# Performance work log

Measured on AMD Instinct MI355X. Metric: run time of the kernel, lower is better.

The kernel has to match this reference:

```python
import jax, jax.numpy as jnp
import numpy as np

K = 8          # opt.pk, explicit precision cutoff
MARGIN = 0.2   # opt.margin
NEG = -1e30    # sentinel for masked sort keys


def setup_inputs() -> dict:
    key = jax.random.key(0)
    k1, k2 = jax.random.split(key)
    batch_reprs = jax.random.normal(k1, (4096, 512), dtype=jnp.float32)
    batch_labels = jax.random.randint(k2, (4096,), 0, 64)
    return {"batch_reprs": batch_reprs, "batch_labels": batch_labels}


def _forward(batch_reprs, batch_labels):
    B = batch_reprs.shape[0]
    dt = batch_reprs.dtype
    # cls_match_mat: 1 if same class
    match = (batch_labels[:, None] == batch_labels[None, :]).astype(dt)
    # pairwise euclidean distance (squared=False), safe sqrt at zero diagonal
    sq = jnp.sum(batch_reprs * batch_reprs, axis=1)
    res = jnp.maximum(sq[:, None] - 2.0 * (batch_reprs @ batch_reprs.T) + sq[None, :], 0.0)
    zero = res <= 0.0
    d = jnp.where(zero, 0.0, jnp.sqrt(jnp.where(zero, 1.0, res)))
    sim_hat = -d + (1.0 - match) * MARGIN  # use_margin=True path
    # rank via double argsort (descending similarity -> rank 1 = best)
    order = jnp.argsort(-sim_hat, axis=1)
    rank = jnp.argsort(order, axis=1).astype(dt) + 1.0
    pos_nums = jnp.sum(match, axis=1)
    ks = jnp.minimum(pos_nums, jnp.asarray(K + 1, dt))[:, None]  # k_mat per row
    w = 1.0 / jnp.log2(rank + 1.0) + 1.0  # DCG-style rank weight
    # false positives: not same class, within top-k_i
    fp_mask = (match < 1.0) & (rank <= ks)
    fp_nums = jnp.sum(fp_mask, axis=1)  # |N| per row
    # false negatives: same class, beyond top-k_i
    fn_mask = (match > 0.0) & (rank > ks)
    fp_term = jnp.sum(jnp.where(fp_mask, sim_hat * w, 0.0))
    # per-row variable-size topk over false negatives, vectorized:
    # mask non-FN entries to -inf, sort desc, keep first fp_nums[i] entries
    fn_key = jnp.where(fn_mask, sim_hat, NEG)
    fn_order = jnp.argsort(-fn_key, axis=1)
    sorted_sim = jnp.take_along_axis(sim_hat, fn_order, axis=1)
    sorted_w = jnp.take_along_axis(w, fn_order, axis=1)
    sorted_valid = jnp.take_along_axis(fn_mask, fn_order, axis=1)
    take = (jnp.arange(B)[None, :].astype(dt) < fp_nums[:, None]) & sorted_valid
    fn_term = jnp.sum(jnp.where(take, sorted_sim * sorted_w, 0.0))
    # rows with fp_num==0 contribute 0 to both terms, matching the host loop
    return fp_term - fn_term


def reference(batch_reprs, batch_labels):
    return _forward(batch_reprs, batch_labels)
```

## Files before the change

### kernel.cpp

```cpp
#include <hip/hip_runtime.h>
#include <math.h>

#define BB 4096
#define DD 512
#define KTOP 9
#define MARGIN_F 0.2f
#define NT 32
#define NTRI (NT * (NT + 1) / 2)

typedef __attribute__((ext_vector_type(8))) short short8;
typedef __attribute__((ext_vector_type(4))) float f32x4;
typedef unsigned long long u64;

__device__ unsigned short g_Rhi[(size_t)BB * DD];
__device__ u64 g_cmask[64 * 64];

__device__ __forceinline__ unsigned short f2bf(float x) {
  unsigned u = __float_as_uint(x);
  u += 0x7fffu + ((u >> 16) & 1u);
  return (unsigned short)(u >> 16);
}

__device__ __forceinline__ float ord16val(unsigned o16) {
  unsigned e = (o16 << 16) | 0x8000u;
  unsigned s = (e & 0x80000000u) ? (e ^ 0x80000000u) : ~e;
  return __uint_as_float(s);
}

__device__ __forceinline__ unsigned wavemax32_dpp(unsigned c) {
#define MSTEP(CTRL, RM)                                                        \
  {                                                                            \
    unsigned o = (unsigned)__builtin_amdgcn_update_dpp(0, (int)c, CTRL, RM, 0xf, false); \
    if (o > c) c = o;                                                          \
  }
  MSTEP(0xB1, 0xf) MSTEP(0x4E, 0xf) MSTEP(0x141, 0xf) MSTEP(0x140, 0xf)
  MSTEP(0x142, 0xa) MSTEP(0x143, 0xc)
#undef MSTEP
  return (unsigned)__builtin_amdgcn_readlane((int)c, 63);
}

__device__ __forceinline__ int wavesum_dpp(int c) {
#define SSTEP(CTRL, RM)                                                        \
  c += __builtin_amdgcn_update_dpp(0, c, CTRL, RM, 0xf, false);
  SSTEP(0xB1, 0xf) SSTEP(0x4E, 0xf) SSTEP(0x141, 0xf) SSTEP(0x140, 0xf)
  SSTEP(0x142, 0xa) SSTEP(0x143, 0xc)
#undef SSTEP
  return __builtin_amdgcn_readlane(c, 63);
}

__device__ __forceinline__ unsigned u4c(const uint4& f, int q) {
  return q == 0 ? f.x : q == 1 ? f.y : q == 2 ? f.z : f.w;
}

__global__ __launch_bounds__(64) void splitsq(const float* __restrict__ R,
                                              float* __restrict__ sq) {
  const int row = blockIdx.x, lane = threadIdx.x;
  const float4* r4 = (const float4*)(R + (size_t)row * DD);
  float4 a = r4[lane], b = r4[lane + 64];
  float xs[8] = {a.x, a.y, a.z, a.w, b.x, b.y, b.z, b.w};
  unsigned short hs[8];
  float s = 0.f;
  #pragma unroll
  for (int q = 0; q < 8; ++q) {
    float x = xs[q];
    s += x * x;
    hs[q] = f2bf(x);
  }
  const size_t base = (size_t)row * DD;
  *(ushort4*)&g_Rhi[base + lane * 4]       = *(ushort4*)&hs[0];
  *(ushort4*)&g_Rhi[base + 256 + lane * 4] = *(ushort4*)&hs[4];
  #pragma unroll
  for (int off = 32; off; off >>= 1) s += __shfl_down(s, off);
  if (lane == 0) sq[row] = s;
}

__global__ __launch_bounds__(64) void buildmask(const int* __restrict__ labels) {
  __shared__ int slab[BB];
  const int c = blockIdx.x, lane = threadIdx.x;
  for (int i = lane; i < BB / 4; i += 64) ((int4*)slab)[i] = ((const int4*)labels)[i];
  __syncthreads();
  u64 m = 0;
  #pragma unroll
  for (int e = 0; e < 64; ++e) {
    int j = 512 * (e >> 3) + 8 * lane + (e & 7);
    m |= (u64)(slab[j] == c) << e;
  }
  g_cmask[c * 64 + lane] = m;
}

__global__ __launch_bounds__(256, 2) void simgemm_rs2(const int* __restrict__ labels,
                                                      const float* __restrict__ sq,
                                                      unsigned short* __restrict__ simq) {
  const int x = blockIdx.x & 7;
  int c = blockIdx.x >> 3;
  int bi = 0, bj = 0;
  #pragma unroll
  for (int q = 0; q < 4; ++q) {
    const int bjq = (q < 2) ? (2 * x + q) : (28 - 2 * x + q);
    const int n = bjq + 1;
    if (c >= 0 && c < n) { bj = bjq; bi = c; }
    c -= n;
  }
  const int i0 = bi * 128, j0 = bj * 128;

  __shared__ __align__(16) unsigned char smembytes[65536];
  unsigned short (*kbuf)[2][8192] = (unsigned short (*)[2][8192])smembytes;

  const int tid = threadIdx.x;
  const int wid = tid >> 6, lane = tid & 63;
  const int wr = wid >> 1, wc = wid & 1;
  const int lrow = lane & 15, kblk = lane >> 4;

  const int sr = lane & 15;
  const int sc = (lane >> 4) * 8;
  const int r0 = (2 * wid + 0) * 16 + sr;
  const int r1 = (2 * wid + 1) * 16 + sr;
  const unsigned short* gA0 = &g_Rhi[(size_t)(i0 + r0) * DD + sc];
  const unsigned short* gA1 = &g_Rhi[(size_t)(i0 + r1) * DD + sc];
  const unsigned short* gB0 = &g_Rhi[(size_t)(j0 + r0) * DD + sc];
  const unsigned short* gB1 = &g_Rhi[(size_t)(j0 + r1) * DD + sc];

  f32x4 acc[4][4] = {};
  uint4 vA00, vA01, vA10, vA11, vB00, vB01, vB10, vB11;

#define STAGE_LOAD(K0)                                                         \
  vA00 = *(const uint4*)(gA0 + (K0));      vB00 = *(const uint4*)(gB0 + (K0)); \
  vA01 = *(const uint4*)(gA0 + (K0) + 32); vB01 = *(const uint4*)(gB0 + (K0) + 32); \
  vA10 = *(const uint4*)(gA1 + (K0));      vB10 = *(const uint4*)(gB1 + (K0)); \
  vA11 = *(const uint4*)(gA1 + (K0) + 32); vB11 = *(const uint4*)(gB1 + (K0) + 32);

#define STAGE_WRITE(BUF)                                                       \
  {                                                                            \
    const int c0 = (2 * wid + 0) * 1024 + lane * 8;                            \
    const int c1 = (2 * wid + 1) * 1024 + lane * 8;                            \
    *(uint4*)&kbuf[BUF][0][c0]       = vA00; *(uint4*)&kbuf[BUF][1][c0]       = vB00; \
    *(uint4*)&kbuf[BUF][0][c0 + 512] = vA01; *(uint4*)&kbuf[BUF][1][c0 + 512] = vB01; \
    *(uint4*)&kbuf[BUF][0][c1]       = vA10; *(uint4*)&kbuf[BUF][1][c1]       = vB10; \
    *(uint4*)&kbuf[BUF][0][c1 + 512] = vA11; *(uint4*)&kbuf[BUF][1][c1 + 512] = vB11; \
  }

  STAGE_LOAD(0);
  STAGE_WRITE(0);
  STAGE_LOAD(64);
  __syncthreads();

  for (int step = 0; step < 8; ++step) {
    const int cur = step & 1;

    #pragma unroll
    for (int kk = 0; kk < 2; ++kk) {
      short8 a[4], b[4];
      #pragma unroll
      for (int m = 0; m < 4; ++m)
        a[m] = *(const short8*)&kbuf[cur][0][(wr * 4 + m) * 1024 + kk * 512 + lane * 8];
      #pragma unroll
      for (int n = 0; n < 4; ++n)
        b[n] = *(const short8*)&kbuf[cur][1][(wc * 4 + n) * 1024 + kk * 512 + lane * 8];
      #pragma unroll
      for (int m = 0; m < 4; ++m) {
        #pragma unroll
        for (int n = 0; n < 4; ++n) {
          acc[m][n] = __builtin_amdgcn_mfma_f32_16x16x32_bf16(a[m], b[n], acc[m][n], 0, 0, 0);
        }
      }
    }

    if (step < 7) {
      STAGE_WRITE(cur ^ 1);
      if (step < 6) { STAGE_LOAD((step + 2) * 64); }
      __syncthreads();
    }
  }
#undef STAGE_LOAD
#undef STAGE_WRITE

  __syncthreads();
  unsigned short (*T)[132] = (unsigned short (*)[132])smembytes;
  float* sqi = (float*)(smembytes + 33792);
  float* sqj = (float*)(smembytes + 34304);
  int* labi  = (int*)(smembytes + 34816);
  int* labj  = (int*)(smembytes + 35328);
  if (tid < 128) { sqi[tid] = sq[i0 + tid]; labi[tid] = labels[i0 + tid]; }
  else { int t2 = tid - 128; sqj[t2] = sq[j0 + t2]; labj[t2] = labels[j0 + t2]; }
  __syncthreads();

  #pragma unroll
  for (int m = 0; m < 4; ++m) {
    const int rbase = wr * 64 + m * 16 + kblk * 4;
    #pragma unroll
    for (int n = 0; n < 4; ++n) {
      const int ccol = wc * 64 + n * 16 + lrow;
      const float sqc = sqj[ccol];
      const int lc_ = labj[ccol];
      #pragma unroll
      for (int reg = 0; reg < 4; ++reg) {
        const int r = rbase + reg;
        float res = sqi[r] - 2.0f * acc[m][n][reg] + sqc;
        float dd = (res <= 0.f) ? 0.f : sqrtf(res);
        float sv = -dd + ((labi[r] != lc_) ? MARGIN_F : 0.f);
        unsigned su = __float_as_uint(sv);
        unsigned ord = su ^ ((unsigned)((int)su >> 31) | 0x80000000u);
        T[r][ccol] = (unsigned short)(ord >> 16);
      }
    }
  }
  __syncthreads();

  const int srow0 = tid >> 4, scol0 = (tid & 15) * 8;
  #pragma unroll
  for (int p = 0; p < 8; ++p) {
    const int r = p * 16 + srow0;
    short8 w = *(const short8*)&T[r][scol0];
    *(short8*)&simq[(size_t)(i0 + r) * BB + j0 + scol0] = w;
  }
  if (bi != bj) {
    #pragma unroll
    for (int p = 0; p < 8; ++p) {
      const int col = p * 16 + srow0;
      unsigned short tmp[8];
      #pragma unroll
      for (int t = 0; t < 8; ++t) tmp[t] = T[scol0 + t][col];
      *(short8*)&simq[(size_t)(j0 + col) * BB + i0 + scol0] = *(short8*)tmp;
    }
  }
}

#define TOP2UPD(k, a, b) {                                                     \
  unsigned _mx = ((k) > (a)) ? (k) : (a);                                      \
  unsigned _mn = ((k) > (a)) ? (a) : (k);                                      \
  (a) = _mx;                                                                   \
  (b) = (_mn > (b)) ? _mn : (b); }

__global__ __launch_bounds__(128) void rowproc9(const unsigned short* __restrict__ simq,
                                                const int* __restrict__ labels,
                                                float* __restrict__ partials) {
  __shared__ unsigned sred[2 * KTOP + 2][2];
  __shared__ int sint[2 + 2 * KTOP];

  const int tid = threadIdx.x;
  const int lane = tid & 63;
  const int h = tid >> 6;
  const int row = blockIdx.x;

  const uint4* rp = (const uint4*)(simq + (size_t)row * BB);
  uint4 w0 = rp[lane + (4 * h + 0) * 64];
  uint4 w1 = rp[lane + (4 * h + 1) * 64];
  uint4 w2 = rp[lane + (4 * h + 2) * 64];
  uint4 w3 = rp[lane + (4 * h + 3) * 64];

  const int myl = labels[row];
  const unsigned mh = (unsigned)(g_cmask[myl * 64 + lane] >> (32 * h));
  const unsigned lbase2 = (unsigned)((4095 - 8 * lane) << 1);

  unsigned k[32];
  #pragma unroll
  for (int s = 0; s < 4; ++s) {
    const uint4 w = s == 0 ? w0 : s == 1 ? w1 : s == 2 ? w2 : w3;
    const unsigned base_s = lbase2 - (unsigned)(1024 * (4 * h + s));
    #pragma unroll
    for (int q = 0; q < 4; ++q) {
      const unsigned wv = u4c(w, q);
      const int e0 = s * 8 + q * 2;
      k[e0]     = ((wv & 0xffffu) << 13)
                | (base_s - (unsigned)((q * 2) << 1)     + ((mh >> e0) & 1u));
      k[e0 + 1] = ((wv >> 16) << 13)
                | (base_s - (unsigned)((q * 2 + 1) << 1) + ((mh >> (e0 + 1)) & 1u));
    }
  }

  {
    int p = wavesum_dpp(__popc(mh));
    sint[h] = p;
  }
  __syncthreads();
  const int pos = sint[0] + sint[1];
  const int ks = min(pos, KTOP);

  unsigned h1 = 0, h2 = 0;
  #pragma unroll
  for (int e = 0; e < 32; ++e) TOP2UPD(k[e], h1, h2);

  unsigned kth = 0;
  float fp = 0.f; int fpn = 0;
  #pragma unroll
  for (int t = 0; t < KTOP; ++t) {
    if (t < ks) {
      sred[t][h] = wavemax32_dpp(h1);
    }
    __syncthreads();
    if (t < ks) {
      const unsigned g = max(sred[t][0], sred[t][1]);
      if (!(g & 1u)) { fp += ord16val(g >> 13) * (1.f / log2f((float)(t + 2)) + 1.f); fpn++; }
      if (t == ks - 1) kth = g;
      if (h1 == g) {
        h1 = h2; h2 = ~0u;
        if (h1 == ~0u) {
          h1 = 0; h2 = 0;
          #pragma unroll
          for (int e = 0; e < 32; ++e) {
            if (k[e] < g) TOP2UPD(k[e], h1, h2);
          }
        }
      }
    }
  }

  float fn = 0.f;
  if (fpn > 0) {
    unsigned f1 = 0, f2 = 0;
    #pragma unroll
    for (int e = 0; e < 32; ++e) {
      if ((k[e] & 1u) && k[e] < kth) TOP2UPD(k[e], f1, f2);
    }
    unsigned ck[KTOP];
    int nc = 0;
    #pragma unroll
    for (int u = 0; u < KTOP; ++u) {
      ck[u] = ~0u;
      if (u < fpn) {
        sred[KTOP + 1 + u][h] = wavemax32_dpp(f1);
      }
      __syncthreads();
      if (u < fpn) {
        const unsigned g = max(sred[KTOP + 1 + u][0], sred[KTOP + 1 + u][1]);
        if (g != 0u) {
          ck[u] = g; nc = u + 1;
          if (f1 == g) {
            f1 = f2; f2 = ~0u;
            if (f1 == ~0u) {
              f1 = 0; f2 = 0;
              #pragma unroll
              for (int e = 0; e < 32; ++e) {
                if ((k[e] & 1u) && k[e] < g) TOP2UPD(k[e], f1, f2);
              }
            }
          }
        }
      }
    }
    if (nc > 0) {
      int cnt[KTOP];
      #pragma unroll
      for (int u = 0; u < KTOP; ++u) cnt[u] = 0;
      #pragma unroll
      for (int e = 0; e < 32; ++e) {
        #pragma unroll
        for (int u = 0; u < KTOP; ++u) cnt[u] += (k[e] > ck[u]) ? 1 : 0;
      }
      #pragma unroll
      for (int u = 0; u < KTOP; ++u) {
        sint[2 + h * KTOP + u] = wavesum_dpp(cnt[u]);
      }
    }
    __syncthreads();
    if (nc > 0) {
      #pragma unroll
      for (int u = 0; u < KTOP; ++u) {
        if (u < nc) {
          const int rank = 1 + sint[2 + u] + sint[2 + KTOP + u];
          fn += ord16val(ck[u] >> 13) * (1.f / log2f((float)(rank + 1)) + 1.f);
        }
      }
    }
  }

  if (tid == 0) partials[row] = fp - fn;
}

__global__ __launch_bounds__(256) void finalreduce(const float* __restrict__ partials,
                                                   float* __restrict__ out) {
  __shared__ float s[256];
  const int tid = threadIdx.x;
  float acc = 0.f;
  for (int j = tid; j < BB; j += 256) acc += partials[j];
  s[tid] = acc; __syncthreads();
  #pragma unroll
  for (int st = 128; st; st >>= 1) { if (tid < st) s[tid] += s[tid + st]; __syncthreads(); }
  if (tid == 0) out[0] = s[0];
}

extern "C" void kernel_launch(void* const* d_in, const int* in_sizes, int n_in,
                              void* d_out, int out_size, void* d_ws, size_t ws_size,
                              hipStream_t stream) {
  const float* R      = (const float*)d_in[0];
  const int*   labels = (const int*)d_in[1];
  float* out = (float*)d_out;

  unsigned short* simq = (unsigned short*)d_ws;
  float* sq            = (float*)((char*)d_ws + (size_t)BB * BB * 2);
  float* partials      = sq + BB;

  splitsq<<<BB, 64, 0, stream>>>(R, sq);
  buildmask<<<64, 64, 0, stream>>>(labels);
  simgemm_rs2<<<NTRI, 256, 0, stream>>>(labels, sq, simq);
  rowproc9<<<BB, 128, 0, stream>>>(simq, labels, partials);
  finalreduce<<<1, 256, 0, stream>>>(partials, out);
}
```

Before: 93.06 us.

## Repack bf16 operands into MFMA fragment layout and load GEMM operands directly from global

Adds a repack kernel that rewrites the bf16 matrix into per-16-row blocks already laid out as MFMA fragments. The similarity GEMM then reads its fragments straight from global memory (cached in L2) with register double-buffering, dropping the LDS staging, the double-buffered shared tiles and the per-step barriers. Shared memory per block shrinks to the size the epilogue needs. The cost is an extra kernel launch and a full extra pass over the bf16 copy, plus reliance on cache hits for operands that are reused across tiles.

```diff
diff --git a/kernel.cpp b/kernel.cpp
--- a/kernel.cpp
+++ b/kernel.cpp
@@ -13,6 +13,7 @@
 typedef unsigned long long u64;
 
 __device__ unsigned short g_Rhi[(size_t)BB * DD];
+__device__ unsigned short g_Rpk[(size_t)BB * DD];
 __device__ u64 g_cmask[64 * 64];
 
 __device__ __forceinline__ unsigned short f2bf(float x) {
@@ -74,6 +75,19 @@
   if (lane == 0) sq[row] = s;
 }
 
+__global__ __launch_bounds__(256) void repack(void) {
+  const int p = blockIdx.x;
+  #pragma unroll
+  for (int i = 0; i < 4; ++i) {
+    const int idx = i * 256 + threadIdx.x;
+    const int ks = idx >> 6, l = idx & 63;
+    const int row = p * 16 + (l & 15);
+    const int k0 = ks * 32 + (l >> 4) * 8;
+    *(uint4*)&g_Rpk[(size_t)p * 8192 + (size_t)idx * 8] =
+        *(const uint4*)&g_Rhi[(size_t)row * DD + k0];
+  }
+}
+
 __global__ __launch_bounds__(64) void buildmask(const int* __restrict__ labels) {
   __shared__ int slab[BB];
   const int c = blockIdx.x, lane = threadIdx.x;
@@ -88,9 +102,9 @@
   g_cmask[c * 64 + lane] = m;
 }
 
-__global__ __launch_bounds__(256, 2) void simgemm_rs2(const int* __restrict__ labels,
-                                                      const float* __restrict__ sq,
-                                                      unsigned short* __restrict__ simq) {
+__global__ __launch_bounds__(256, 2) void simgemm_pk(const int* __restrict__ labels,
+                                                     const float* __restrict__ sq,
+                                                     unsigned short* __restrict__ simq) {
   const int x = blockIdx.x & 7;
   int c = blockIdx.x >> 3;
   int bi = 0, bj = 0;
@@ -103,78 +117,50 @@
   }
   const int i0 = bi * 128, j0 = bj * 128;
 
-  __shared__ __align__(16) unsigned char smembytes[65536];
-  unsigned short (*kbuf)[2][8192] = (unsigned short (*)[2][8192])smembytes;
+  __shared__ __align__(16) unsigned char smembytes[35840];
 
   const int tid = threadIdx.x;
   const int wid = tid >> 6, lane = tid & 63;
   const int wr = wid >> 1, wc = wid & 1;
   const int lrow = lane & 15, kblk = lane >> 4;
 
-  const int sr = lane & 15;
-  const int sc = (lane >> 4) * 8;
-  const int r0 = (2 * wid + 0) * 16 + sr;
-  const int r1 = (2 * wid + 1) * 16 + sr;
-  const unsigned short* gA0 = &g_Rhi[(size_t)(i0 + r0) * DD + sc];
-  const unsigned short* gA1 = &g_Rhi[(size_t)(i0 + r1) * DD + sc];
-  const unsigned short* gB0 = &g_Rhi[(size_t)(j0 + r0) * DD + sc];
-  const unsigned short* gB1 = &g_Rhi[(size_t)(j0 + r1) * DD + sc];
+  const unsigned short* pA[4];
+  const unsigned short* pB[4];
+  #pragma unroll
+  for (int m = 0; m < 4; ++m) {
+    pA[m] = g_Rpk + (size_t)(bi * 8 + wr * 4 + m) * 8192 + lane * 8;
+    pB[m] = g_Rpk + (size_t)(bj * 8 + wc * 4 + m) * 8192 + lane * 8;
+  }
 
   f32x4 acc[4][4] = {};
-  uint4 vA00, vA01, vA10, vA11, vB00, vB01, vB10, vB11;
-
-#define STAGE_LOAD(K0)                                                         \
-  vA00 = *(const uint4*)(gA0 + (K0));      vB00 = *(const uint4*)(gB0 + (K0)); \
-  vA01 = *(const uint4*)(gA0 + (K0) + 32); vB01 = *(const uint4*)(gB0 + (K0) + 32); \
-  vA10 = *(const uint4*)(gA1 + (K0));      vB10 = *(const uint4*)(gB1 + (K0)); \
-  vA11 = *(const uint4*)(gA1 + (K0) + 32); vB11 = *(const uint4*)(gB1 + (K0) + 32);
-
-#define STAGE_WRITE(BUF)                                                       \
-  {                                                                            \
-    const int c0 = (2 * wid + 0) * 1024 + lane * 8;                            \
-    const int c1 = (2 * wid + 1) * 1024 + lane * 8;                            \
-    *(uint4*)&kbuf[BUF][0][c0]       = vA00; *(uint4*)&kbuf[BUF][1][c0]       = vB00; \
-    *(uint4*)&kbuf[BUF][0][c0 + 512] = vA01; *(uint4*)&kbuf[BUF][1][c0 + 512] = vB01; \
-    *(uint4*)&kbuf[BUF][0][c1]       = vA10; *(uint4*)&kbuf[BUF][1][c1]       = vB10; \
-    *(uint4*)&kbuf[BUF][0][c1 + 512] = vA11; *(uint4*)&kbuf[BUF][1][c1 + 512] = vB11; \
-  }
-
-  STAGE_LOAD(0);
-  STAGE_WRITE(0);
-  STAGE_LOAD(64);
-  __syncthreads();
-
-  for (int step = 0; step < 8; ++step) {
+  short8 fa[2][4], fb[2][4];
+
+  #pragma unroll
+  for (int m = 0; m < 4; ++m) {
+    fa[0][m] = *(const short8*)(pA[m]);
+    fb[0][m] = *(const short8*)(pB[m]);
+  }
+
+  #pragma unroll
+  for (int step = 0; step < 16; ++step) {
     const int cur = step & 1;
-
-    #pragma unroll
-    for (int kk = 0; kk < 2; ++kk) {
-      short8 a[4], b[4];
-      #pragma unroll
-      for (int m = 0; m < 4; ++m)
-        a[m] = *(const short8*)&kbuf[cur][0][(wr * 4 + m) * 1024 + kk * 512 + lane * 8];
-      #pragma unroll
-      for (int n = 0; n < 4; ++n)
-        b[n] = *(const short8*)&kbuf[cur][1][(wc * 4 + n) * 1024 + kk * 512 + lane * 8];
+    if (step < 15) {
+      const int koff = (step + 1) * 512;
       #pragma unroll
       for (int m = 0; m < 4; ++m) {
-        #pragma unroll
-        for (int n = 0; n < 4; ++n) {
-          acc[m][n] = __builtin_amdgcn_mfma_f32_16x16x32_bf16(a[m], b[n], acc[m][n], 0, 0, 0);
-        }
-      }
-    }
-
-    if (step < 7) {
-      STAGE_WRITE(cur ^ 1);
-      if (step < 6) { STAGE_LOAD((step + 2) * 64); }
-      __syncthreads();
-    }
-  }
-#undef STAGE_LOAD
-#undef STAGE_WRITE
-
-  __syncthreads();
+        fa[cur ^ 1][m] = *(const short8*)(pA[m] + koff);
+        fb[cur ^ 1][m] = *(const short8*)(pB[m] + koff);
+      }
+    }
+    #pragma unroll
+    for (int m = 0; m < 4; ++m) {
+      #pragma unroll
+      for (int n = 0; n < 4; ++n) {
+        acc[m][n] = __builtin_amdgcn_mfma_f32_16x16x32_bf16(fa[cur][m], fb[cur][n], acc[m][n], 0, 0, 0);
+      }
+    }
+  }
+
   unsigned short (*T)[132] = (unsigned short (*)[132])smembytes;
   float* sqi = (float*)(smembytes + 33792);
   float* sqj = (float*)(smembytes + 34304);
@@ -391,8 +377,9 @@
   float* partials      = sq + BB;
 
   splitsq<<<BB, 64, 0, stream>>>(R, sq);
+  repack<<<BB / 16, 256, 0, stream>>>();
   buildmask<<<64, 64, 0, stream>>>(labels);
-  simgemm_rs2<<<NTRI, 256, 0, stream>>>(labels, sq, simq);
+  simgemm_pk<<<NTRI, 256, 0, stream>>>(labels, sq, simq);
   rowproc9<<<BB, 128, 0, stream>>>(simq, labels, partials);
   finalreduce<<<1, 256, 0, stream>>>(partials, out);
 }
```

Measured after the change: 89.08 us. -4.3%, faster.
